# Kernel tuning notes

Measured on AMD Instinct MI355X. Metric: run time of the kernel, lower is better.

The kernel has to match this reference:

```python
import jax, jax.numpy as jnp
import numpy as np

NUM_HEADS = 4

def setup_inputs() -> dict:
    key = jax.random.key(0)
    ks = jax.random.split(key, 5)
    B, N, C = 2, 4096, 256
    s = 0.02
    return {
        "x": jax.random.normal(ks[0], (B, N, C), dtype=jnp.float32),
        "qkv_w": jax.random.normal(ks[1], (3 * C, C), dtype=jnp.float32) * s,
        "qkv_b": jax.random.normal(ks[2], (3 * C,), dtype=jnp.float32) * s,
        "out_w": jax.random.normal(ks[3], (C, C), dtype=jnp.float32) * s,
        "out_b": jax.random.normal(ks[4], (C,), dtype=jnp.float32) * s,
    }

def reference(x, qkv_w, qkv_b, out_w, out_b):
    # x: [B, N, C]; manual multi-head self-attention (eval mode, dropout off)
    B, N, C = x.shape
    H = NUM_HEADS
    D = C // H
    qkv = x @ qkv_w.T + qkv_b                      # [B, N, 3C]
    qkv = qkv.reshape(B, N, 3, H, D)
    qkv = jnp.transpose(qkv, (2, 0, 3, 1, 4))      # [3, B, H, N, D]
    q, k, v = qkv[0], qkv[1], qkv[2]
    scale = D ** -0.5
    attn = jnp.einsum('bhnd,bhmd->bhnm', q, k) * scale  # [B, H, N, N]
    attn = jax.nn.softmax(attn, axis=-1)
    out = jnp.einsum('bhnm,bhmd->bhnd', attn, v)   # [B, H, N, D]
    out = jnp.transpose(out, (0, 2, 1, 3)).reshape(B, N, C)
    return out @ out_w.T + out_b
```

## Files before the change

### kernel.cpp

```cpp
#include <hip/hip_runtime.h>

typedef __bf16 bf16x8 __attribute__((ext_vector_type(8)));
typedef float f32x4 __attribute__((ext_vector_type(4)));

#define MFMA_BF16(a, b, c) __builtin_amdgcn_mfma_f32_16x16x32_bf16((a), (b), (c), 0, 0, 0)

#define C1 0.18033688f

static __device__ __forceinline__ unsigned short f2bf(float f) {
    unsigned int u = __float_as_uint(f);
    unsigned int r = (u + 0x7fffu + ((u >> 16) & 1u)) >> 16;
    return (unsigned short)r;
}
static __device__ __forceinline__ float bf2f(unsigned short us) {
    return __uint_as_float(((unsigned int)us) << 16);
}
static __device__ __forceinline__ float exp2_hw(float x) {
    float r;
    asm("v_exp_f32 %0, %1" : "=v"(r) : "v"(x));
    return r;
}
static __device__ __forceinline__ unsigned pack_rh(float a, float b) {
    return __byte_perm(__float_as_uint(a) + 0x8000u, __float_as_uint(b) + 0x8000u, 0x7632);
}
static __device__ __forceinline__ void gload16(const void* g, void* l) {
    __builtin_amdgcn_global_load_lds(
        (const __attribute__((address_space(1))) unsigned int*)g,
        (__attribute__((address_space(3))) unsigned int*)l, 16, 0, 0);
}

template <bool QKV>
__global__ __launch_bounds__(256) void gemm_kernel(
    const void* __restrict__ Av, const void* __restrict__ Wv,
    const void* __restrict__ biasv, unsigned short* __restrict__ Cb,
    float* __restrict__ Cf, unsigned short* __restrict__ Vt, int Nout) {
    constexpr int K = 256;
    __shared__ __align__(16) char sm[32768];

    const int tid = threadIdx.x;
    const int lane = tid & 63;
    const int wv = tid >> 6;
    const int m16 = lane & 15;
    const int quad = lane >> 4;
    const int bm = blockIdx.x * 64;
    const int bn = blockIdx.y * 64;

    int cnt = 0;
    {
        const unsigned short* sw = (const unsigned short*)Wv;
#pragma unroll
        for (int i = 0; i < 4; i++) {
            const int e = (sw[i * 64 + lane] >> 7) & 0xFF;
            cnt += __popcll(__ballot(e >= 195));
        }
    }
    const bool f32 = (cnt >= 8);

    int bgo[2], blo[2], brow[2], bchk[2];
#pragma unroll
    for (int i = 0; i < 2; i++) {
        const int c = wv * 128 + i * 64 + lane;
        const int r = c >> 3, g = (c & 7) ^ (r & 7);
        bgo[i] = r * (K * 2) + g * 16;
        blo[i] = c * 16;
        brow[i] = r;
        bchk[i] = g;
    }
    int bro[4][2];
#pragma unroll
    for (int t = 0; t < 4; t++)
#pragma unroll
        for (int ks = 0; ks < 2; ks++) {
            const int row = t * 16 + m16;
            bro[t][ks] = row * 64 + ((4 * ks + quad) ^ (m16 & 7)) * 8;
        }

    bf16x8 a[4][2];
    if (f32) {
        const float* Wf = (const float*)Wv;
#pragma unroll
        for (int kb = 0; kb < 4; kb++)
#pragma unroll
            for (int i = 0; i < 2; i++) {
                const float* src = Wf + (size_t)(bn + brow[i]) * K + kb * 64 + bchk[i] * 8;
                const float4 u0 = *(const float4*)src;
                const float4 u1 = *(const float4*)(src + 4);
                uint4 p;
                p.x = pack_rh(u0.x, u0.y);
                p.y = pack_rh(u0.z, u0.w);
                p.z = pack_rh(u1.x, u1.y);
                p.w = pack_rh(u1.z, u1.w);
                *(uint4*)(sm + kb * 8192 + blo[i]) = p;
            }
    } else {
        const char* bg = (const char*)Wv + (size_t)bn * K * 2;
#pragma unroll
        for (int kb = 0; kb < 4; kb++)
#pragma unroll
            for (int i = 0; i < 2; i++)
                gload16(bg + kb * 128 + bgo[i], sm + kb * 8192 + blo[i]);
    }
    if (QKV && f32) {
        const float* Af = (const float*)Av + (size_t)(bm + wv * 16 + m16) * K + quad * 8;
#pragma unroll
        for (int kb = 0; kb < 4; kb++)
#pragma unroll
            for (int ks = 0; ks < 2; ks++) {
                const float4 u0 = *(const float4*)(Af + kb * 64 + ks * 32);
                const float4 u1 = *(const float4*)(Af + kb * 64 + ks * 32 + 4);
                uint4 p;
                p.x = pack_rh(u0.x, u0.y);
                p.y = pack_rh(u0.z, u0.w);
                p.z = pack_rh(u1.x, u1.y);
                p.w = pack_rh(u1.z, u1.w);
                a[kb][ks] = *(const bf16x8*)&p;
            }
    } else {
        const unsigned short* ap =
            (const unsigned short*)Av + (size_t)(bm + wv * 16 + m16) * K + quad * 8;
#pragma unroll
        for (int kb = 0; kb < 4; kb++)
#pragma unroll
            for (int ks = 0; ks < 2; ks++)
                a[kb][ks] = *(const bf16x8*)(ap + kb * 64 + ks * 32);
    }

    __syncthreads();

    f32x4 acc[4] = {};
#pragma unroll
    for (int kb = 0; kb < 4; kb++) {
        const unsigned short* Blds = (const unsigned short*)(sm + kb * 8192);
#pragma unroll
        for (int ks = 0; ks < 2; ks++)
#pragma unroll
            for (int t = 0; t < 4; t++) {
                const bf16x8 b = *(const bf16x8*)(Blds + bro[t][ks]);
                acc[t] = MFMA_BF16(a[kb][ks], b, acc[t]);
            }
    }

    const float* bf_ = (const float*)biasv;
    const unsigned short* bh_ = (const unsigned short*)biasv;

    if (QKV && bn >= 512) {
        __syncthreads();
        unsigned short* tr = (unsigned short*)sm;
        const int lr = wv * 16 + quad * 4;
#pragma unroll
        for (int t = 0; t < 4; t++) {
            const int col = bn + t * 16 + m16;
            const float bv = f32 ? bf_[col] : bf2f(bh_[col]);
            uint2 w;
            w.x = pack_rh(acc[t][0] + bv, acc[t][1] + bv);
            w.y = pack_rh(acc[t][2] + bv, acc[t][3] + bv);
            *(uint2*)&tr[(t * 16 + m16) * 72 + lr] = w;
        }
        __syncthreads();
        const int d = tid >> 2;
        const int ch = (tid & 3) * 16;
        const uint4 o4a = *(const uint4*)&tr[d * 72 + ch];
        const uint4 o4b = *(const uint4*)&tr[d * 72 + ch + 8];
        const int hh = (bn - 512) >> 6;
        const int bb = bm >> 12, n0 = bm & 4095;
        const int nn = n0 + ch;
        const int kt = nn >> 7, koff = nn & 127;
        unsigned short* vdst =
            &Vt[(size_t)(((bb * 4 + hh) * 32 + kt) * 64 + d) * 128 + koff];
        *(uint4*)(vdst) = o4a;
        *(uint4*)(vdst + 8) = o4b;
        return;
    }

    const int row0 = bm + wv * 16 + quad * 4;
#pragma unroll
    for (int t = 0; t < 4; t++) {
        const int col = bn + t * 16 + m16;
        const float bv = f32 ? bf_[col] : bf2f(bh_[col]);
        float v[4];
#pragma unroll
        for (int r = 0; r < 4; r++) v[r] = acc[t][r] + bv;
        if (QKV) {
            const float sc = (col < 256) ? C1 : 1.0f;
#pragma unroll
            for (int r = 0; r < 4; r++)
                Cb[(size_t)(row0 + r) * 768 + col] = f2bf(v[r] * sc);
        } else {
            if (f32) {
#pragma unroll
                for (int r = 0; r < 4; r++) Cf[(size_t)(row0 + r) * Nout + col] = v[r];
            } else {
#pragma unroll
                for (int r = 0; r < 4; r++) Cb[(size_t)(row0 + r) * Nout + col] = f2bf(v[r]);
            }
        }
    }
}

#define ZERO_S(S)                                                     \
    do {                                                              \
        _Pragma("unroll") for (int mb = 0; mb < 2; mb++)              \
            _Pragma("unroll") for (int j = 0; j < 4; j++)             \
                S[mb][j] = (f32x4){0.f, 0.f, 0.f, 0.f};               \
    } while (0)

#define QKT(S, KBASE)                                                          \
    do {                                                                       \
        const unsigned short* Kb_ = (const unsigned short*)(KBASE);            \
        __builtin_amdgcn_s_setprio(1);                                         \
        _Pragma("unroll") for (int mb = 0; mb < 2; mb++)                       \
            _Pragma("unroll") for (int ks = 0; ks < 2; ks++) {                 \
                const bf16x8 ka_ = *(const bf16x8*)(Kb_ + kro[mb][ks]);        \
                _Pragma("unroll") for (int j = 0; j < 4; j++)                  \
                    S[mb][j] = MFMA_BF16(ka_, qf[j][ks], S[mb][j]);            \
            }                                                                  \
        __builtin_amdgcn_s_setprio(0);                                         \
    } while (0)

#define EXPP(S, PA)                                                            \
    do {                                                                       \
        _Pragma("unroll") for (int j = 0; j < 4; j++) {                        \
            const float e0 = exp2_hw(S[0][j][0]);                              \
            const float e1 = exp2_hw(S[0][j][1]);                              \
            const float e2 = exp2_hw(S[0][j][2]);                              \
            const float e3 = exp2_hw(S[0][j][3]);                              \
            const float e4 = exp2_hw(S[1][j][0]);                              \
            const float e5 = exp2_hw(S[1][j][1]);                              \
            const float e6 = exp2_hw(S[1][j][2]);                              \
            const float e7 = exp2_hw(S[1][j][3]);                              \
            uint4 pw_;                                                         \
            pw_.x = pack_rh(e0, e1);                                           \
            pw_.y = pack_rh(e2, e3);                                           \
            pw_.z = pack_rh(e4, e5);                                           \
            pw_.w = pack_rh(e6, e7);                                           \
            PA[j] = *(const bf16x8*)&pw_;                                      \
        }                                                                      \
    } while (0)

#define PVACC(PA, VBASE)                                                       \
    do {                                                                       \
        const unsigned short* Vb_ = (const unsigned short*)(VBASE);            \
        __builtin_amdgcn_s_setprio(1);                                         \
        _Pragma("unroll") for (int j = 0; j < 4; j++)                          \
            o1[j] = MFMA_BF16(PA[j], ones, o1[j]);                             \
        _Pragma("unroll") for (int t = 0; t < 4; t++) {                        \
            const uint2 va_ = *(const uint2*)(Vb_ + vroA[t]);                  \
            const uint2 vc_ = *(const uint2*)(Vb_ + (vroA[t] ^ 16));           \
            uint4 vv_;                                                         \
            vv_.x = va_.x;                                                     \
            vv_.y = va_.y;                                                     \
            vv_.z = vc_.x;                                                     \
            vv_.w = vc_.y;                                                     \
            const bf16x8 vb_ = *(const bf16x8*)&vv_;                           \
            _Pragma("unroll") for (int j = 0; j < 4; j++)                      \
                o[j][t] = MFMA_BF16(PA[j], vb_, o[j][t]);                      \
        }                                                                      \
        __builtin_amdgcn_s_setprio(0);                                         \
    } while (0)

#define GLK(DST)                                                               \
    {                                                                          \
        _Pragma("unroll") for (int i = 0; i < 4; i++)                          \
            gload16(kgn + kgo[i], (DST) + klo[i]);                             \
        kgn += 196608;                                                         \
    }
#define GLV(DST)                                                               \
    {                                                                          \
        _Pragma("unroll") for (int i = 0; i < 4; i++)                          \
            gload16(vgn + vgo[i], (DST) + vlo[i]);                             \
        vgn += 16384;                                                          \
    }

__global__ __launch_bounds__(256, 2) void attn_kernel(
    const unsigned short* __restrict__ qkv, const unsigned short* __restrict__ Vt,
    unsigned short* __restrict__ attn, int iters) {
    const int N = 4096, C3 = 768;
    __shared__ __align__(16) char sm[65536];

    const int tid = threadIdx.x;
    const int lane = tid & 63;
    const int wv = tid >> 6;
    const int m16 = lane & 15;
    const int quad = lane >> 4;

    const int bh = blockIdx.x & 7;
    const int qt = blockIdx.x >> 3;
    const int b = bh >> 2, h = bh & 3;

    bf16x8 qf[4][2];
#pragma unroll
    for (int j = 0; j < 4; j++)
#pragma unroll
        for (int ks = 0; ks < 2; ks++)
            qf[j][ks] = *(const bf16x8*)(qkv + ((size_t)b * N + qt * 64 + j * 16 + m16) * C3 +
                                         h * 64 + ks * 32 + quad * 8);

    uint4 ones_u;
    ones_u.x = ones_u.y = ones_u.z = ones_u.w = 0x3F803F80u;
    const bf16x8 ones = *(const bf16x8*)&ones_u;

    int kgo[4], vgo[4], klo[4], vlo[4];
#pragma unroll
    for (int i = 0; i < 4; i++) {
        const int c = i * 64 + lane;
        const int r = c >> 3, g = (c & 7) ^ (r & 7);
        kgo[i] = (wv * 32 + r) * 1536 + g * 16;
        klo[i] = c * 16;
        const int d = c >> 2, js = c & 3, jg = js ^ ((d >> 2) & 3);
        vgo[i] = d * 256 + wv * 64 + jg * 16;
        vlo[i] = c * 16;
    }
    int kro[2][2];
#pragma unroll
    for (int mb = 0; mb < 2; mb++)
#pragma unroll
        for (int ks = 0; ks < 2; ks++) {
            const int row = mb * 16 + m16;
            kro[mb][ks] = row * 64 + ((4 * ks + quad) ^ (m16 & 7)) * 8;
        }
    int vroA[4];
#pragma unroll
    for (int t = 0; t < 4; t++) {
        const int d = t * 16 + m16;
        const int c0 = (quad >> 1) ^ ((d >> 2) & 3);
        vroA[t] = d * 32 + c0 * 8 + (quad & 1) * 4;
    }

    char* Kreg0 = sm + wv * 8192;
    char* Vreg0 = sm + 32768 + wv * 8192;

    const char* kgp = (const char*)(qkv + (size_t)b * N * C3 + 256 + h * 64);
    const char* vgp = (const char*)(Vt + (size_t)bh * 262144);

#pragma unroll
    for (int i = 0; i < 4; i++) gload16(kgp + kgo[i], Kreg0 + klo[i]);
#pragma unroll
    for (int i = 0; i < 4; i++) gload16(vgp + vgo[i], Vreg0 + vlo[i]);
#pragma unroll
    for (int i = 0; i < 4; i++) gload16(kgp + 196608 + kgo[i], Kreg0 + 4096 + klo[i]);
#pragma unroll
    for (int i = 0; i < 4; i++) gload16(vgp + 16384 + vgo[i], Vreg0 + 4096 + vlo[i]);
    const char* kgn = kgp + 2 * 196608;
    const char* vgn = vgp + 2 * 16384;

    f32x4 o[4][4] = {};
    f32x4 o1[4] = {};
    f32x4 sA[2][4], sB[2][4];
    bf16x8 pa[4];

    asm volatile("s_waitcnt vmcnt(12)" ::: "memory");
    ZERO_S(sA);
    QKT(sA, Kreg0);

    for (int t2 = 0; t2 < 15; ++t2) {
        asm volatile("s_waitcnt vmcnt(4)" ::: "memory");
        GLK(Kreg0);
        ZERO_S(sB);
        QKT(sB, Kreg0 + 4096);
        EXPP(sA, pa);
        PVACC(pa, Vreg0);
        asm volatile("s_waitcnt lgkmcnt(0)" ::: "memory");
        GLV(Vreg0);

        asm volatile("s_waitcnt vmcnt(4)" ::: "memory");
        GLK(Kreg0 + 4096);
        ZERO_S(sA);
        QKT(sA, Kreg0);
        EXPP(sB, pa);
        PVACC(pa, Vreg0 + 4096);
        asm volatile("s_waitcnt lgkmcnt(0)" ::: "memory");
        GLV(Vreg0 + 4096);
    }
    asm volatile("s_waitcnt vmcnt(4)" ::: "memory");
    ZERO_S(sB);
    QKT(sB, Kreg0 + 4096);
    EXPP(sA, pa);
    PVACC(pa, Vreg0);
    asm volatile("s_waitcnt vmcnt(0)" ::: "memory");
    EXPP(sB, pa);
    PVACC(pa, Vreg0 + 4096);

    __syncthreads();
    float* Ored = (float*)sm;
    float* lsum = (float*)(sm + 16384);
    if (m16 == 0) {
#pragma unroll
        for (int j = 0; j < 4; j++)
#pragma unroll
            for (int r = 0; r < 4; r++)
                lsum[wv * 64 + j * 16 + quad * 4 + r] = o1[j][r];
    }
    const int row = tid >> 4;
    const int col = (tid & 15) * 4;
#pragma unroll
    for (int j = 0; j < 4; j++) {
#pragma unroll
        for (int t = 0; t < 4; t++)
#pragma unroll
            for (int r = 0; r < 4; r++)
                Ored[(wv * 16 + quad * 4 + r) * 64 + t * 16 + m16] = o[j][t][r];
        __syncthreads();
        f32x4 sum = *(f32x4*)&Ored[row * 64 + col];
        sum += *(f32x4*)&Ored[1024 + row * 64 + col];
        sum += *(f32x4*)&Ored[2048 + row * 64 + col];
        sum += *(f32x4*)&Ored[3072 + row * 64 + col];
        const float lq = lsum[j * 16 + row] + lsum[64 + j * 16 + row] +
                         lsum[128 + j * 16 + row] + lsum[192 + j * 16 + row];
        const int n = qt * 64 + j * 16 + row;
        const float inv = 1.0f / lq;
        uint2 w;
        w.x = pack_rh(sum[0] * inv, sum[1] * inv);
        w.y = pack_rh(sum[2] * inv, sum[3] * inv);
        *(uint2*)&attn[((size_t)b * N + n) * 256 + h * 64 + col] = w;
        __syncthreads();
    }
}

extern "C" void kernel_launch(void* const* d_in, const int* in_sizes, int n_in,
                              void* d_out, int out_size, void* d_ws, size_t ws_size,
                              hipStream_t stream) {
    const int B = 2, N = 4096, H = 4;
    const int M = B * N;

    char* wsb = (char*)d_ws;
    unsigned short* qkv_ws  = (unsigned short*)wsb;
    unsigned short* Vt_ws   = qkv_ws + 6291456;
    unsigned short* attn_ws = Vt_ws + 2097152;

    gemm_kernel<true><<<dim3(M / 64, 768 / 64), 256, 0, stream>>>(
        d_in[0], d_in[1], d_in[2], qkv_ws, nullptr, Vt_ws, 768);

    attn_kernel<<<512, 256, 0, stream>>>(qkv_ws, Vt_ws, attn_ws, 32);

    gemm_kernel<false><<<dim3(M / 64, 256 / 64), 256, 0, stream>>>(
        attn_ws, d_in[3], d_in[4], (unsigned short*)d_out, (float*)d_out, nullptr, 256);
}
```

Baseline: 136.1 us.

## Pre-convert x to bf16 and double-buffer weight staging in GEMM

```diff
diff --git a/kernel.cpp b/kernel.cpp
--- a/kernel.cpp
+++ b/kernel.cpp
@@ -29,13 +29,41 @@
         (__attribute__((address_space(3))) unsigned int*)l, 16, 0, 0);
 }
 
+__global__ __launch_bounds__(256) void convert_x_kernel(
+    const void* __restrict__ x, unsigned short* __restrict__ xb) {
+    const int lane = threadIdx.x & 63;
+    int cnt = 0;
+    {
+        const unsigned short* sx = (const unsigned short*)x;
+#pragma unroll
+        for (int i = 0; i < 4; i++) {
+            const int e = (sx[i * 64 + lane] >> 7) & 0xFF;
+            cnt += __popcll(__ballot(e >= 195));
+        }
+    }
+    const bool f32 = (cnt >= 8);
+    const int base = blockIdx.x * 2048 + (int)threadIdx.x * 8;
+    if (f32) {
+        const float4 u0 = *(const float4*)((const float*)x + base);
+        const float4 u1 = *(const float4*)((const float*)x + base + 4);
+        uint4 p;
+        p.x = pack_rh(u0.x, u0.y);
+        p.y = pack_rh(u0.z, u0.w);
+        p.z = pack_rh(u1.x, u1.y);
+        p.w = pack_rh(u1.z, u1.w);
+        *(uint4*)(xb + base) = p;
+    } else {
+        *(uint4*)(xb + base) = *(const uint4*)((const unsigned short*)x + base);
+    }
+}
+
 template <bool QKV>
 __global__ __launch_bounds__(256) void gemm_kernel(
-    const void* __restrict__ Av, const void* __restrict__ Wv,
+    const unsigned short* __restrict__ A, const void* __restrict__ Wv,
     const void* __restrict__ biasv, unsigned short* __restrict__ Cb,
     float* __restrict__ Cf, unsigned short* __restrict__ Vt, int Nout) {
     constexpr int K = 256;
-    __shared__ __align__(16) char sm[32768];
+    __shared__ __align__(16) char sm[16384];
 
     const int tid = threadIdx.x;
     const int lane = tid & 63;
@@ -75,11 +103,12 @@
             bro[t][ks] = row * 64 + ((4 * ks + quad) ^ (m16 & 7)) * 8;
         }
 
-    bf16x8 a[4][2];
-    if (f32) {
-        const float* Wf = (const float*)Wv;
-#pragma unroll
-        for (int kb = 0; kb < 4; kb++)
+    const char* bg = (const char*)Wv + (size_t)bn * K * 2;
+    const float* Wf = (const float*)Wv;
+    const unsigned short* ap = A + (size_t)(bm + wv * 16 + m16) * K + quad * 8;
+
+    auto stageB = [&](int kb, int buf) {
+        if (f32) {
 #pragma unroll
             for (int i = 0; i < 2; i++) {
                 const float* src = Wf + (size_t)(bn + brow[i]) * K + kb * 64 + bchk[i] * 8;
@@ -90,54 +119,44 @@
                 p.y = pack_rh(u0.z, u0.w);
                 p.z = pack_rh(u1.x, u1.y);
                 p.w = pack_rh(u1.z, u1.w);
-                *(uint4*)(sm + kb * 8192 + blo[i]) = p;
+                *(uint4*)(sm + buf * 8192 + blo[i]) = p;
             }
-    } else {
-        const char* bg = (const char*)Wv + (size_t)bn * K * 2;
-#pragma unroll
-        for (int kb = 0; kb < 4; kb++)
+        } else {
 #pragma unroll
             for (int i = 0; i < 2; i++)
-                gload16(bg + kb * 128 + bgo[i], sm + kb * 8192 + blo[i]);
-    }
-    if (QKV && f32) {
-        const float* Af = (const float*)Av + (size_t)(bm + wv * 16 + m16) * K + quad * 8;
-#pragma unroll
-        for (int kb = 0; kb < 4; kb++)
-#pragma unroll
-            for (int ks = 0; ks < 2; ks++) {
-                const float4 u0 = *(const float4*)(Af + kb * 64 + ks * 32);
-                const float4 u1 = *(const float4*)(Af + kb * 64 + ks * 32 + 4);
-                uint4 p;
-                p.x = pack_rh(u0.x, u0.y);
-                p.y = pack_rh(u0.z, u0.w);
-                p.z = pack_rh(u1.x, u1.y);
-                p.w = pack_rh(u1.z, u1.w);
-                a[kb][ks] = *(const bf16x8*)&p;
-            }
-    } else {
-        const unsigned short* ap =
-            (const unsigned short*)Av + (size_t)(bm + wv * 16 + m16) * K + quad * 8;
-#pragma unroll
-        for (int kb = 0; kb < 4; kb++)
-#pragma unroll
-            for (int ks = 0; ks < 2; ks++)
-                a[kb][ks] = *(const bf16x8*)(ap + kb * 64 + ks * 32);
-    }
-
-    __syncthreads();
+                gload16(bg + kb * 128 + bgo[i], sm + buf * 8192 + blo[i]);
+        }
+    };
+
+    stageB(0, 0);
+    bf16x8 a0 = *(const bf16x8*)(ap);
+    bf16x8 a1 = *(const bf16x8*)(ap + 32);
 
     f32x4 acc[4] = {};
 #pragma unroll
     for (int kb = 0; kb < 4; kb++) {
-        const unsigned short* Blds = (const unsigned short*)(sm + kb * 8192);
-#pragma unroll
-        for (int ks = 0; ks < 2; ks++)
+        __syncthreads();
+        const int cur = kb & 1;
+        bf16x8 a0n, a1n;
+        if (kb < 3) {
+            stageB(kb + 1, cur ^ 1);
+            a0n = *(const bf16x8*)(ap + (kb + 1) * 64);
+            a1n = *(const bf16x8*)(ap + (kb + 1) * 64 + 32);
+        }
+        const unsigned short* Blds = (const unsigned short*)(sm + cur * 8192);
+#pragma unroll
+        for (int ks = 0; ks < 2; ks++) {
+            const bf16x8 a = ks ? a1 : a0;
 #pragma unroll
             for (int t = 0; t < 4; t++) {
                 const bf16x8 b = *(const bf16x8*)(Blds + bro[t][ks]);
-                acc[t] = MFMA_BF16(a[kb][ks], b, acc[t]);
+                acc[t] = MFMA_BF16(a, b, acc[t]);
             }
+        }
+        if (kb < 3) {
+            a0 = a0n;
+            a1 = a1n;
+        }
     }
 
     const float* bf_ = (const float*)biasv;
@@ -423,12 +442,15 @@
     const int M = B * N;
 
     char* wsb = (char*)d_ws;
-    unsigned short* qkv_ws  = (unsigned short*)wsb;
+    unsigned short* xb      = (unsigned short*)wsb;
+    unsigned short* qkv_ws  = xb + 2097152;
     unsigned short* Vt_ws   = qkv_ws + 6291456;
     unsigned short* attn_ws = Vt_ws + 2097152;
 
+    convert_x_kernel<<<1024, 256, 0, stream>>>(d_in[0], xb);
+
     gemm_kernel<true><<<dim3(M / 64, 768 / 64), 256, 0, stream>>>(
-        d_in[0], d_in[1], d_in[2], qkv_ws, nullptr, Vt_ws, 768);
+        xb, d_in[1], d_in[2], qkv_ws, nullptr, Vt_ws, 768);
 
     attn_kernel<<<512, 256, 0, stream>>>(qkv_ws, Vt_ws, attn_ws, 32);
 
```

New measurement: 133.8 us. No clear change (-1.7%).

## Widen QKV GEMM tiles to reuse A fragments and double-buffer B staging

Applied to the files above, without the earlier changes.

```diff
diff --git a/kernel.cpp b/kernel.cpp
--- a/kernel.cpp
+++ b/kernel.cpp
@@ -29,13 +29,14 @@
         (__attribute__((address_space(3))) unsigned int*)l, 16, 0, 0);
 }
 
-template <bool QKV>
+template <bool QKV, int NSUB>
 __global__ __launch_bounds__(256) void gemm_kernel(
     const void* __restrict__ Av, const void* __restrict__ Wv,
     const void* __restrict__ biasv, unsigned short* __restrict__ Cb,
     float* __restrict__ Cf, unsigned short* __restrict__ Vt, int Nout) {
     constexpr int K = 256;
-    __shared__ __align__(16) char sm[32768];
+    constexpr int NP = NSUB * 4;
+    __shared__ __align__(16) char sm[16384];
 
     const int tid = threadIdx.x;
     const int lane = tid & 63;
@@ -43,7 +44,7 @@
     const int m16 = lane & 15;
     const int quad = lane >> 4;
     const int bm = blockIdx.x * 64;
-    const int bn = blockIdx.y * 64;
+    const int bn0 = blockIdx.y * (NSUB * 64);
 
     int cnt = 0;
     {
@@ -75,14 +76,14 @@
             bro[t][ks] = row * 64 + ((4 * ks + quad) ^ (m16 & 7)) * 8;
         }
 
-    bf16x8 a[4][2];
-    if (f32) {
-        const float* Wf = (const float*)Wv;
-#pragma unroll
-        for (int kb = 0; kb < 4; kb++)
+    const float* Wf = (const float*)Wv;
+
+    auto stageB = [&](int sub, int kb, int buf) {
+        if (f32) {
 #pragma unroll
             for (int i = 0; i < 2; i++) {
-                const float* src = Wf + (size_t)(bn + brow[i]) * K + kb * 64 + bchk[i] * 8;
+                const float* src =
+                    Wf + (size_t)(bn0 + sub * 64 + brow[i]) * K + kb * 64 + bchk[i] * 8;
                 const float4 u0 = *(const float4*)src;
                 const float4 u1 = *(const float4*)(src + 4);
                 uint4 p;
@@ -90,16 +91,18 @@
                 p.y = pack_rh(u0.z, u0.w);
                 p.z = pack_rh(u1.x, u1.y);
                 p.w = pack_rh(u1.z, u1.w);
-                *(uint4*)(sm + kb * 8192 + blo[i]) = p;
+                *(uint4*)(sm + buf * 8192 + blo[i]) = p;
             }
-    } else {
-        const char* bg = (const char*)Wv + (size_t)bn * K * 2;
-#pragma unroll
-        for (int kb = 0; kb < 4; kb++)
+        } else {
+            const char* bgs = (const char*)Wv + (size_t)(bn0 + sub * 64) * K * 2;
 #pragma unroll
             for (int i = 0; i < 2; i++)
-                gload16(bg + kb * 128 + bgo[i], sm + kb * 8192 + blo[i]);
-    }
+                gload16(bgs + kb * 128 + bgo[i], sm + buf * 8192 + blo[i]);
+        }
+    };
+
+    stageB(0, 0, 0);
+    bf16x8 a[4][2];
     if (QKV && f32) {
         const float* Af = (const float*)Av + (size_t)(bm + wv * 16 + m16) * K + quad * 8;
 #pragma unroll
@@ -125,74 +128,86 @@
                 a[kb][ks] = *(const bf16x8*)(ap + kb * 64 + ks * 32);
     }
 
-    __syncthreads();
-
-    f32x4 acc[4] = {};
-#pragma unroll
-    for (int kb = 0; kb < 4; kb++) {
-        const unsigned short* Blds = (const unsigned short*)(sm + kb * 8192);
+    f32x4 acc[NSUB][4] = {};
+#pragma unroll
+    for (int p = 0; p < NP; p++) {
+        __syncthreads();
+        const int cur = p & 1;
+        if (p + 1 < NP) stageB((p + 1) >> 2, (p + 1) & 3, cur ^ 1);
+        const unsigned short* Blds = (const unsigned short*)(sm + cur * 8192);
+        const int sub = p >> 2, kb = p & 3;
 #pragma unroll
         for (int ks = 0; ks < 2; ks++)
 #pragma unroll
             for (int t = 0; t < 4; t++) {
                 const bf16x8 b = *(const bf16x8*)(Blds + bro[t][ks]);
-                acc[t] = MFMA_BF16(a[kb][ks], b, acc[t]);
+                acc[sub][t] = MFMA_BF16(a[kb][ks], b, acc[sub][t]);
             }
     }
 
     const float* bf_ = (const float*)biasv;
     const unsigned short* bh_ = (const unsigned short*)biasv;
-
-    if (QKV && bn >= 512) {
-        __syncthreads();
-        unsigned short* tr = (unsigned short*)sm;
-        const int lr = wv * 16 + quad * 4;
+    const int row0 = bm + wv * 16 + quad * 4;
+
+#pragma unroll
+    for (int sub = 0; sub < NSUB; sub++) {
+        const int ct = bn0 + sub * 64;
+        if (QKV && ct >= 512) continue;
 #pragma unroll
         for (int t = 0; t < 4; t++) {
-            const int col = bn + t * 16 + m16;
+            const int col = ct + t * 16 + m16;
             const float bv = f32 ? bf_[col] : bf2f(bh_[col]);
-            uint2 w;
-            w.x = pack_rh(acc[t][0] + bv, acc[t][1] + bv);
-            w.y = pack_rh(acc[t][2] + bv, acc[t][3] + bv);
-            *(uint2*)&tr[(t * 16 + m16) * 72 + lr] = w;
-        }
-        __syncthreads();
-        const int d = tid >> 2;
-        const int ch = (tid & 3) * 16;
-        const uint4 o4a = *(const uint4*)&tr[d * 72 + ch];
-        const uint4 o4b = *(const uint4*)&tr[d * 72 + ch + 8];
-        const int hh = (bn - 512) >> 6;
-        const int bb = bm >> 12, n0 = bm & 4095;
-        const int nn = n0 + ch;
-        const int kt = nn >> 7, koff = nn & 127;
-        unsigned short* vdst =
-            &Vt[(size_t)(((bb * 4 + hh) * 32 + kt) * 64 + d) * 128 + koff];
-        *(uint4*)(vdst) = o4a;
-        *(uint4*)(vdst + 8) = o4b;
-        return;
-    }
-
-    const int row0 = bm + wv * 16 + quad * 4;
-#pragma unroll
-    for (int t = 0; t < 4; t++) {
-        const int col = bn + t * 16 + m16;
-        const float bv = f32 ? bf_[col] : bf2f(bh_[col]);
-        float v[4];
-#pragma unroll
-        for (int r = 0; r < 4; r++) v[r] = acc[t][r] + bv;
-        if (QKV) {
-            const float sc = (col < 256) ? C1 : 1.0f;
-#pragma unroll
-            for (int r = 0; r < 4; r++)
-                Cb[(size_t)(row0 + r) * 768 + col] = f2bf(v[r] * sc);
-        } else {
-            if (f32) {
-#pragma unroll
-                for (int r = 0; r < 4; r++) Cf[(size_t)(row0 + r) * Nout + col] = v[r];
+            float v[4];
+#pragma unroll
+            for (int r = 0; r < 4; r++) v[r] = acc[sub][t][r] + bv;
+            if (QKV) {
+                const float sc = (col < 256) ? C1 : 1.0f;
+#pragma unroll
+                for (int r = 0; r < 4; r++)
+                    Cb[(size_t)(row0 + r) * 768 + col] = f2bf(v[r] * sc);
             } else {
-#pragma unroll
-                for (int r = 0; r < 4; r++) Cb[(size_t)(row0 + r) * Nout + col] = f2bf(v[r]);
+                if (f32) {
+#pragma unroll
+                    for (int r = 0; r < 4; r++) Cf[(size_t)(row0 + r) * Nout + col] = v[r];
+                } else {
+#pragma unroll
+                    for (int r = 0; r < 4; r++)
+                        Cb[(size_t)(row0 + r) * Nout + col] = f2bf(v[r]);
+                }
             }
+        }
+    }
+
+    if (QKV) {
+#pragma unroll
+        for (int sub = 0; sub < NSUB; sub++) {
+            const int ct = bn0 + sub * 64;
+            if (ct < 512) continue;
+            __syncthreads();
+            unsigned short* tr = (unsigned short*)sm;
+            const int lr = wv * 16 + quad * 4;
+#pragma unroll
+            for (int t = 0; t < 4; t++) {
+                const int col = ct + t * 16 + m16;
+                const float bv = f32 ? bf_[col] : bf2f(bh_[col]);
+                uint2 w;
+                w.x = pack_rh(acc[sub][t][0] + bv, acc[sub][t][1] + bv);
+                w.y = pack_rh(acc[sub][t][2] + bv, acc[sub][t][3] + bv);
+                *(uint2*)&tr[(t * 16 + m16) * 72 + lr] = w;
+            }
+            __syncthreads();
+            const int d = tid >> 2;
+            const int ch = (tid & 3) * 16;
+            const uint4 o4a = *(const uint4*)&tr[d * 72 + ch];
+            const uint4 o4b = *(const uint4*)&tr[d * 72 + ch + 8];
+            const int hh = (ct - 512) >> 6;
+            const int bb = bm >> 12, n0 = bm & 4095;
+            const int nn = n0 + ch;
+            const int kt = nn >> 7, koff = nn & 127;
+            unsigned short* vdst =
+                &Vt[(size_t)(((bb * 4 + hh) * 32 + kt) * 64 + d) * 128 + koff];
+            *(uint4*)(vdst) = o4a;
+            *(uint4*)(vdst + 8) = o4b;
         }
     }
 }
@@ -427,11 +442,11 @@
     unsigned short* Vt_ws   = qkv_ws + 6291456;
     unsigned short* attn_ws = Vt_ws + 2097152;
 
-    gemm_kernel<true><<<dim3(M / 64, 768 / 64), 256, 0, stream>>>(
+    gemm_kernel<true, 3><<<dim3(M / 64, 4), 256, 0, stream>>>(
         d_in[0], d_in[1], d_in[2], qkv_ws, nullptr, Vt_ws, 768);
 
     attn_kernel<<<512, 256, 0, stream>>>(qkv_ws, Vt_ws, attn_ws, 32);
 
-    gemm_kernel<false><<<dim3(M / 64, 256 / 64), 256, 0, stream>>>(
+    gemm_kernel<false, 1><<<dim3(M / 64, 4), 256, 0, stream>>>(
         attn_ws, d_in[3], d_in[4], (unsigned short*)d_out, (float*)d_out, nullptr, 256);
 }
```

Measured after the change: 135.7 us. About the same (-0.3%).
